# Kernel tuning notes

Hardware: AMD Instinct MI355X
Metric: run time of the kernel (lower is better)

Reference implementation:

```python
import jax, jax.numpy as jnp
import numpy as np

B, N, D = 16, 2048, 64

def setup_inputs() -> dict:
    key = jax.random.key(0)
    kq, kk, kv = jax.random.split(key, 3)
    q = jax.random.normal(kq, (B, N, D), dtype=jnp.float32)
    k = jax.random.normal(kk, (B, N, D), dtype=jnp.float32)
    v = jax.random.normal(kv, (B, N, D), dtype=jnp.float32)
    scale = jnp.float32(1.0 / np.sqrt(D))  # canonical 1/sqrt(d_head)
    return {"q": q, "k": k, "v": v, "scale": scale}

def reference(q, k, v, scale):
    # attention = softmax((q @ k^T) * scale) over key axis; dropout p=0.0 is identity
    scores = jnp.einsum('bqd,bkd->bqk', q, k) * scale  # [B,N,N]
    attention = jax.nn.softmax(scores, axis=2)
    context = jnp.einsum('bqk,bkd->bqd', attention, v)  # [B,N,D]
    return (context, attention)
```

## Files before the change

### kernel.cpp

```cpp
#include <hip/hip_runtime.h>

#define Bb 16
#define Nn 2048
#define Dd 64

typedef __attribute__((ext_vector_type(8))) short s16x8;
typedef __attribute__((ext_vector_type(4))) short s16x4;
typedef __attribute__((ext_vector_type(4))) float fx4;

__device__ __forceinline__ unsigned short f2bf(float f) {
  union { float f; unsigned u; } v; v.f = f;
  unsigned r = v.u + 0x7FFFu + ((v.u >> 16) & 1u);
  return (unsigned short)(r >> 16);
}

__global__ void k_cvtK(const float* __restrict__ K, unsigned short* __restrict__ Kb) {
  int i = blockIdx.x * 256 + threadIdx.x;
  float4 f = ((const float4*)K)[i];
  ushort4 o;
  o.x = f2bf(f.x); o.y = f2bf(f.y); o.z = f2bf(f.z); o.w = f2bf(f.w);
  ((ushort4*)Kb)[i] = o;
}

__global__ void k_transV(const float* __restrict__ V, unsigned short* __restrict__ VT) {
  __shared__ float tile[32][33];
  int b = blockIdx.z;
  int j0 = blockIdx.x * 32, d0 = blockIdx.y * 32;
  int tx = threadIdx.x, ty = threadIdx.y;
  const float* Vb = V + (size_t)b * Nn * Dd;
  unsigned short* Tb = VT + (size_t)b * Dd * Nn;
  for (int r = ty; r < 32; r += 8)
    tile[r][tx] = Vb[(size_t)(j0 + r) * Dd + d0 + tx];
  __syncthreads();
  for (int r = ty; r < 32; r += 8)
    Tb[(size_t)(d0 + r) * Nn + j0 + tx] = f2bf(tile[tx][r]);
}

__global__ __launch_bounds__(256) void k_attn(
    const float* __restrict__ Q, const unsigned short* __restrict__ Kbf,
    const unsigned short* __restrict__ VTbf, const float* __restrict__ scale_p,
    float* __restrict__ ctx, float* att) {
  const int b = blockIdx.y;
  const int q0 = blockIdx.x * 64;
  const int tid = threadIdx.x;
  const int wave = tid >> 6, lane = tid & 63;
  const int nl = lane & 15, quad = lane >> 4;
  const int qrow = q0 + wave * 16 + nl;
  const float c2 = scale_p[0] * 1.44269504088896341f;

  s16x8 qb[2];
  {
    const float* qp = Q + ((size_t)b * Nn + qrow) * Dd + quad * 8;
#pragma unroll
    for (int kt = 0; kt < 2; ++kt) {
      float4 f0 = *(const float4*)(qp + kt * 32);
      float4 f1 = *(const float4*)(qp + kt * 32 + 4);
      s16x8 t;
      t[0] = (short)f2bf(f0.x); t[1] = (short)f2bf(f0.y);
      t[2] = (short)f2bf(f0.z); t[3] = (short)f2bf(f0.w);
      t[4] = (short)f2bf(f1.x); t[5] = (short)f2bf(f1.y);
      t[6] = (short)f2bf(f1.z); t[7] = (short)f2bf(f1.w);
      qb[kt] = t;
    }
  }
  const unsigned short* Kb = Kbf + (size_t)b * Nn * Dd;
  const unsigned short* VTb = VTbf + (size_t)b * Dd * Nn;
  float* attb = att + (size_t)b * Nn * Nn;

  float m = -3.0e38f, l = 0.0f;

  for (int t = 0; t < 16; ++t) {
    const int k0 = t * 128;
    fx4 s[8];
#pragma unroll
    for (int nt = 0; nt < 8; ++nt) s[nt] = (fx4){0.f, 0.f, 0.f, 0.f};
#pragma unroll
    for (int nt = 0; nt < 8; ++nt) {
      const s16x8* ka =
          (const s16x8*)(Kb + ((size_t)(k0 + nt * 16 + nl)) * Dd + quad * 8);
      s[nt] = __builtin_amdgcn_mfma_f32_16x16x32_bf16(ka[0], qb[0], s[nt], 0, 0, 0);
      s[nt] = __builtin_amdgcn_mfma_f32_16x16x32_bf16(ka[4], qb[1], s[nt], 0, 0, 0);
    }
    float lm = s[0][0];
#pragma unroll
    for (int nt = 0; nt < 8; ++nt)
#pragma unroll
      for (int r = 0; r < 4; ++r) lm = fmaxf(lm, s[nt][r]);
    float mn = fmaxf(m, lm * c2);
    float ls = 0.f;
#pragma unroll
    for (int nt = 0; nt < 8; ++nt)
#pragma unroll
      for (int r = 0; r < 4; ++r) ls += exp2f(fmaf(s[nt][r], c2, -mn));
    l = l * exp2f(m - mn) + ls;
    m = mn;
  }
#pragma unroll
  for (int mask = 16; mask <= 32; mask <<= 1) {
    float om = __shfl_xor(m, mask, 64);
    float ol = __shfl_xor(l, mask, 64);
    float mn = fmaxf(m, om);
    l = l * exp2f(m - mn) + ol * exp2f(om - mn);
    m = mn;
  }
  const float rinv = 1.0f / l;

  fx4 o[4];
#pragma unroll
  for (int d = 0; d < 4; ++d) o[d] = (fx4){0.f, 0.f, 0.f, 0.f};

  for (int t = 0; t < 16; ++t) {
    const int k0 = t * 128;
    fx4 s[8];
#pragma unroll
    for (int nt = 0; nt < 8; ++nt) s[nt] = (fx4){0.f, 0.f, 0.f, 0.f};
#pragma unroll
    for (int nt = 0; nt < 8; ++nt) {
      const s16x8* ka =
          (const s16x8*)(Kb + ((size_t)(k0 + nt * 16 + nl)) * Dd + quad * 8);
      s[nt] = __builtin_amdgcn_mfma_f32_16x16x32_bf16(ka[0], qb[0], s[nt], 0, 0, 0);
      s[nt] = __builtin_amdgcn_mfma_f32_16x16x32_bf16(ka[4], qb[1], s[nt], 0, 0, 0);
    }
#pragma unroll
    for (int nt = 0; nt < 8; ++nt) {
      fx4 p;
#pragma unroll
      for (int r = 0; r < 4; ++r)
        p[r] = exp2f(fmaf(s[nt][r], c2, -m)) * rinv;
      *(fx4*)(attb + (size_t)qrow * Nn + k0 + nt * 16 + quad * 4) = p;
      s16x4 pa;
      pa[0] = (short)f2bf(p[0]); pa[1] = (short)f2bf(p[1]);
      pa[2] = (short)f2bf(p[2]); pa[3] = (short)f2bf(p[3]);
#pragma unroll
      for (int ntd = 0; ntd < 4; ++ntd) {
        s16x4 vb = *(const s16x4*)(VTb + ((size_t)(ntd * 16 + nl)) * Nn + k0 +
                                   nt * 16 + quad * 4);
        o[ntd] = __builtin_amdgcn_mfma_f32_16x16x16bf16_1k(pa, vb, o[ntd], 0, 0, 0);
      }
    }
  }
#pragma unroll
  for (int ntd = 0; ntd < 4; ++ntd)
#pragma unroll
    for (int r = 0; r < 4; ++r)
      ctx[((size_t)b * Nn + q0 + wave * 16 + quad * 4 + r) * Dd + ntd * 16 + nl] =
          o[ntd][r];
}

extern "C" void kernel_launch(void* const* d_in, const int* in_sizes, int n_in,
                              void* d_out, int out_size, void* d_ws, size_t ws_size,
                              hipStream_t stream) {
  const float* q = (const float*)d_in[0];
  const float* k = (const float*)d_in[1];
  const float* v = (const float*)d_in[2];
  const float* scale = (const float*)d_in[3];

  float* ctx = (float*)d_out;
  float* att = ctx + (size_t)Bb * Nn * Dd;

  unsigned short* Kbf = (unsigned short*)d_ws;
  unsigned short* VTbf = Kbf + (size_t)Bb * Nn * Dd;

  hipLaunchKernelGGL(k_cvtK, dim3((Bb * Nn * Dd) / (256 * 4)), dim3(256), 0, stream,
                     k, Kbf);
  hipLaunchKernelGGL(k_transV, dim3(Nn / 32, Dd / 32, Bb), dim3(32, 8), 0, stream,
                     v, VTbf);
  hipLaunchKernelGGL(k_attn, dim3(Nn / 64, Bb), dim3(256), 0, stream,
                     q, Kbf, VTbf, scale, ctx, att);
}
```

Baseline: 546.6 us.

## Split key range across waves per 16-row block with LDS merge and XCD swizzle

Each block now handles 16 query rows, and its four waves split the key axis four ways. They combine softmax max and sum statistics through shared memory, then reduce partial context outputs in LDS. The grid grows to 2048 one-dimensional blocks with a block-id swizzle, apparently so each XCD works on contiguous batches for K/V cache locality. V loads are hoisted ahead of the exp computation. This adds two barriers and LDS traffic but raises parallelism and may improve L2 reuse.

```diff
diff --git a/kernel.cpp b/kernel.cpp
--- a/kernel.cpp
+++ b/kernel.cpp
@@ -40,13 +40,20 @@
     const float* __restrict__ Q, const unsigned short* __restrict__ Kbf,
     const unsigned short* __restrict__ VTbf, const float* __restrict__ scale_p,
     float* __restrict__ ctx, float* att) {
-  const int b = blockIdx.y;
-  const int q0 = blockIdx.x * 64;
+  const int id = blockIdx.x;
+  const int swz = ((id & 7) << 8) | (id >> 3);
+  const int b = swz >> 7;
+  const int q0 = (swz & 127) << 4;
+
   const int tid = threadIdx.x;
   const int wave = tid >> 6, lane = tid & 63;
   const int nl = lane & 15, quad = lane >> 4;
-  const int qrow = q0 + wave * 16 + nl;
+  const int qrow = q0 + nl;
   const float c2 = scale_p[0] * 1.44269504088896341f;
+
+  __shared__ float sm[4][16];
+  __shared__ float sl[4][16];
+  __shared__ float ob[4][16][64];
 
   s16x8 qb[2];
   {
@@ -69,8 +76,8 @@
 
   float m = -3.0e38f, l = 0.0f;
 
-  for (int t = 0; t < 16; ++t) {
-    const int k0 = t * 128;
+  for (int t = 0; t < 4; ++t) {
+    const int k0 = (wave * 4 + t) * 128;
     fx4 s[8];
 #pragma unroll
     for (int nt = 0; nt < 8; ++nt) s[nt] = (fx4){0.f, 0.f, 0.f, 0.f};
@@ -103,14 +110,28 @@
     l = l * exp2f(m - mn) + ol * exp2f(om - mn);
     m = mn;
   }
-  const float rinv = 1.0f / l;
+  if (lane < 16) { sm[wave][lane] = m; sl[wave][lane] = l; }
+  __syncthreads();
+  float rinv;
+  {
+    float M = sm[0][nl], L = sl[0][nl];
+#pragma unroll
+    for (int j = 1; j < 4; ++j) {
+      float mj = sm[j][nl], lj = sl[j][nl];
+      float mn = fmaxf(M, mj);
+      L = L * exp2f(M - mn) + lj * exp2f(mj - mn);
+      M = mn;
+    }
+    m = M;
+    rinv = 1.0f / L;
+  }
 
   fx4 o[4];
 #pragma unroll
   for (int d = 0; d < 4; ++d) o[d] = (fx4){0.f, 0.f, 0.f, 0.f};
 
-  for (int t = 0; t < 16; ++t) {
-    const int k0 = t * 128;
+  for (int t = 0; t < 4; ++t) {
+    const int k0 = (wave * 4 + t) * 128;
     fx4 s[8];
 #pragma unroll
     for (int nt = 0; nt < 8; ++nt) s[nt] = (fx4){0.f, 0.f, 0.f, 0.f};
@@ -123,6 +144,11 @@
     }
 #pragma unroll
     for (int nt = 0; nt < 8; ++nt) {
+      s16x4 vb[4];
+#pragma unroll
+      for (int ntd = 0; ntd < 4; ++ntd)
+        vb[ntd] = *(const s16x4*)(VTb + ((size_t)(ntd * 16 + nl)) * Nn + k0 +
+                                  nt * 16 + quad * 4);
       fx4 p;
 #pragma unroll
       for (int r = 0; r < 4; ++r)
@@ -132,19 +158,28 @@
       pa[0] = (short)f2bf(p[0]); pa[1] = (short)f2bf(p[1]);
       pa[2] = (short)f2bf(p[2]); pa[3] = (short)f2bf(p[3]);
 #pragma unroll
-      for (int ntd = 0; ntd < 4; ++ntd) {
-        s16x4 vb = *(const s16x4*)(VTb + ((size_t)(ntd * 16 + nl)) * Nn + k0 +
-                                   nt * 16 + quad * 4);
-        o[ntd] = __builtin_amdgcn_mfma_f32_16x16x16bf16_1k(pa, vb, o[ntd], 0, 0, 0);
-      }
-    }
-  }
+      for (int ntd = 0; ntd < 4; ++ntd)
+        o[ntd] = __builtin_amdgcn_mfma_f32_16x16x16bf16_1k(pa, vb[ntd], o[ntd], 0, 0, 0);
+    }
+  }
+
 #pragma unroll
   for (int ntd = 0; ntd < 4; ++ntd)
 #pragma unroll
     for (int r = 0; r < 4; ++r)
-      ctx[((size_t)b * Nn + q0 + wave * 16 + quad * 4 + r) * Dd + ntd * 16 + nl] =
-          o[ntd][r];
+      ob[wave][quad * 4 + r][ntd * 16 + nl] = o[ntd][r];
+  __syncthreads();
+  {
+    const int row = tid >> 4;
+    const int col = (tid & 15) << 2;
+    fx4 a = *(const fx4*)&ob[0][row][col];
+#pragma unroll
+    for (int j = 1; j < 4; ++j) {
+      fx4 tt = *(const fx4*)&ob[j][row][col];
+      a[0] += tt[0]; a[1] += tt[1]; a[2] += tt[2]; a[3] += tt[3];
+    }
+    *(fx4*)(ctx + ((size_t)b * Nn + q0 + row) * Dd + col) = a;
+  }
 }
 
 extern "C" void kernel_launch(void* const* d_in, const int* in_sizes, int n_in,
@@ -165,6 +200,6 @@
                      k, Kbf);
   hipLaunchKernelGGL(k_transV, dim3(Nn / 32, Dd / 32, Bb), dim3(32, 8), 0, stream,
                      v, VTbf);
-  hipLaunchKernelGGL(k_attn, dim3(Nn / 64, Bb), dim3(256), 0, stream,
+  hipLaunchKernelGGL(k_attn, dim3(Bb * Nn / 16), dim3(256), 0, stream,
                      q, Kbf, VTbf, scale, ctx, att);
 }
```

Result: faster. 493.1 us (-9.8%).
